# Kernel tuning notes

Measured on AMD Instinct MI355X. Metric: run time of the kernel, lower is better.

Reference implementation:

```python
import jax, jax.numpy as jnp
import numpy as np

N_E = 1024      # codes per sub-codebook
E_DIM = 64      # code dimension
BETA = 0.25     # commitment cost (VectorQuantizer(n_e, e_dim, 0.25))


def setup_inputs() -> dict:
    key = jax.random.key(0)
    k1, k2 = jax.random.split(key)
    bs, c, h, w = 16, 512, 32, 32
    m = c // E_DIM  # 8 sub-codebooks
    z = jax.random.normal(k1, (bs, c, h, w), dtype=jnp.float32)
    # taming-style init: uniform(-1/n_e, 1/n_e)
    codebooks = jax.random.uniform(
        k2, (m, N_E, E_DIM), dtype=jnp.float32,
        minval=-1.0 / N_E, maxval=1.0 / N_E)
    return {"z": z, "codebooks": codebooks}


def reference(z, codebooks):
    bs, c, h, w = z.shape
    m, n_e, e_dim = codebooks.shape
    N = bs * h * w
    # [bs,c,h,w] -> [bs,h,w,c] -> [m, N, e_dim]: batched over all m sub-codebooks at once
    zf = z.transpose(0, 2, 3, 1).reshape(N, m, e_dim).transpose(1, 0, 2)

    # squared L2 distances: ||z||^2 + ||e||^2 - 2 z.e   -> [m, N, n_e]
    d = ((zf ** 2).sum(-1, keepdims=True)
         + (codebooks ** 2).sum(-1)[:, None, :]
         - 2.0 * jnp.einsum('mnd,mkd->mnk', zf, codebooks))
    idx = jnp.argmin(d, axis=-1)  # [m, N]

    # gather nearest codes: [m, N, e_dim]
    zq = jnp.take_along_axis(codebooks, idx[:, :, None], axis=1)

    # per-sub-codebook VQ loss, summed over m (loss = sum(loss_list))
    codebook_loss = jnp.mean((jax.lax.stop_gradient(zq) - zf) ** 2, axis=(1, 2))
    commit_loss = jnp.mean((zq - jax.lax.stop_gradient(zf)) ** 2, axis=(1, 2))
    loss = jnp.sum(codebook_loss + BETA * commit_loss)

    # straight-through estimator
    zq_st = zf + jax.lax.stop_gradient(zq - zf)

    # reassemble: [m,N,d] -> [N,m*d] -> [bs,h,w,c] -> [bs,c,h,w]
    z_vq = zq_st.transpose(1, 0, 2).reshape(bs, h, w, c).transpose(0, 3, 1, 2)

    # concat of per-codebook index tensors along dim 0
    min_encoding_indices = idx.reshape(-1)  # [m*N]
    # per-code occupancy counts summed over the m codebooks -> [n_e]
    bin_count = jnp.zeros((n_e,), jnp.int32).at[min_encoding_indices].add(1)

    return z_vq, loss, min_encoding_indices, bin_count
```

## Files before the change

kernel.cpp:

```cpp
#include <hip/hip_runtime.h>
#include <cfloat>

#define BS 16
#define CC 512
#define HWD 1024
#define NN 16384
#define MM 8
#define NE 1024
#define ED 64

#define LOSS_OFF 8388608
#define IDX_OFF  8388609
#define BIN_OFF  8519681

#define TAU 4e-5f
#define UWIN 400u

#define WS_B     0
#define WS_IDX   32768
#define WS_CNT   557056
#define WS_LIST  557088
#define WS_OF    688160
#define WS_CAND  720928
#define WS_BMAT  3866656

typedef __attribute__((ext_vector_type(8))) short bf16x8;
typedef __attribute__((ext_vector_type(16))) float f32x16;

__device__ __forceinline__ unsigned short f2bf(float f) {
    unsigned int u = __float_as_uint(f);
    unsigned int r = (u + 0x7fffu + ((u >> 16) & 1u)) >> 16;
    return (unsigned short)r;
}
__device__ __forceinline__ float bf2f(unsigned short h) {
    return __uint_as_float(((unsigned int)h) << 16);
}
__device__ __forceinline__ unsigned umin_(unsigned a, unsigned b) { return a < b ? a : b; }
__device__ __forceinline__ unsigned umax_(unsigned a, unsigned b) { return a > b ? a : b; }
__device__ __forceinline__ unsigned umin3(unsigned a, unsigned b, unsigned c) {
    return umin_(umin_(a, b), c);
}

__device__ __forceinline__ float mul_rn(float a, float b) {
#pragma clang fp contract(off)
    return a * b;
}
__device__ __forceinline__ float add_rn(float a, float b) {
#pragma clang fp contract(off)
    return a + b;
}
__device__ __forceinline__ float sub_rn(float a, float b) {
#pragma clang fp contract(off)
    return a - b;
}

__device__ __forceinline__ float np_sumsq64(const float* x) {
    float r[8];
#pragma unroll
    for (int j = 0; j < 8; ++j) r[j] = mul_rn(x[j], x[j]);
#pragma unroll
    for (int i = 8; i < 64; i += 8) {
#pragma unroll
        for (int j = 0; j < 8; ++j) r[j] = add_rn(r[j], mul_rn(x[i + j], x[i + j]));
    }
    return add_rn(add_rn(add_rn(r[0], r[1]), add_rn(r[2], r[3])),
                  add_rn(add_rn(r[4], r[5]), add_rn(r[6], r[7])));
}

__device__ __forceinline__ float np_dot64(const float* zsh, const float4* cr4) {
    float v0 = 0.f, v1 = 0.f, v2 = 0.f, v3 = 0.f;
#pragma unroll
    for (int t = 0; t < 4; ++t) {
        float4 e0 = cr4[t * 4 + 0];
        float4 e1 = cr4[t * 4 + 1];
        float4 e2 = cr4[t * 4 + 2];
        float4 e3 = cr4[t * 4 + 3];
        const int d0 = 16 * t;
        v0 = add_rn(mul_rn(zsh[d0 + 0], e0.x),
             add_rn(mul_rn(zsh[d0 + 4], e1.x),
             add_rn(mul_rn(zsh[d0 + 8], e2.x),
             add_rn(mul_rn(zsh[d0 + 12], e3.x), v0))));
        v1 = add_rn(mul_rn(zsh[d0 + 1], e0.y),
             add_rn(mul_rn(zsh[d0 + 5], e1.y),
             add_rn(mul_rn(zsh[d0 + 9], e2.y),
             add_rn(mul_rn(zsh[d0 + 13], e3.y), v1))));
        v2 = add_rn(mul_rn(zsh[d0 + 2], e0.z),
             add_rn(mul_rn(zsh[d0 + 6], e1.z),
             add_rn(mul_rn(zsh[d0 + 10], e2.z),
             add_rn(mul_rn(zsh[d0 + 14], e3.z), v2))));
        v3 = add_rn(mul_rn(zsh[d0 + 3], e0.w),
             add_rn(mul_rn(zsh[d0 + 7], e1.w),
             add_rn(mul_rn(zsh[d0 + 11], e2.w),
             add_rn(mul_rn(zsh[d0 + 15], e3.w), v3))));
    }
    return add_rn(add_rn(v0, v1), add_rn(v2, v3));
}

__global__ __launch_bounds__(256) void prep_kernel(const float* __restrict__ cb,
                                                   float* __restrict__ Bhat,
                                                   uint4* __restrict__ Bmat,
                                                   float* __restrict__ out,
                                                   int* __restrict__ cnt) {
    const int tid = threadIdx.x;
    if (blockIdx.x < 32) {
        int i = blockIdx.x * 256 + tid;
        if (i == 0) { out[LOSS_OFF] = 0.0f; cnt[0] = 0; cnt[1] = 0; }
        if (i < NE) out[BIN_OFF + i] = 0.0f;
        const float4* r4 = (const float4*)(cb + (size_t)i * ED);
        float x[ED];
#pragma unroll
        for (int q = 0; q < 16; ++q) {
            float4 v = r4[q];
            x[q*4+0] = v.x; x[q*4+1] = v.y; x[q*4+2] = v.z; x[q*4+3] = v.w;
        }
        Bhat[i] = np_sumsq64(x);
        return;
    }
    int t = (blockIdx.x - 32) * 256 + tid;
    int lane = t & 63;
    int ct = (t >> 6) & 31;
    int rem = t >> 11;
    int c = rem % 13;
    int m = rem / 13;
    int h = lane >> 5;
    int k = ct * 32 + (lane & 31);

    unsigned short v[8];
#pragma unroll
    for (int j = 0; j < 8; ++j) v[j] = 0;

    if (c < 12) {
        int d0 = 16 * (c & 3) + 8 * h;
        const float* e = cb + ((size_t)m * NE + k) * ED + d0;
#pragma unroll
        for (int j = 0; j < 8; ++j) {
            float f = -2.0f * e[j];
            unsigned short hi = f2bf(f);
            v[j] = (c >= 4 && c < 8) ? f2bf(f - bf2f(hi)) : hi;
        }
    } else if (h == 0) {
        const float* e = cb + ((size_t)m * NE + k) * ED;
        float s = 0.f;
#pragma unroll
        for (int d = 0; d < ED; ++d) s += e[d] * e[d];
        v[0] = f2bf(s);
        v[1] = 0x3F80;
    }
    uint4 o;
    o.x = (unsigned)v[0] | ((unsigned)v[1] << 16);
    o.y = (unsigned)v[2] | ((unsigned)v[3] << 16);
    o.z = (unsigned)v[4] | ((unsigned)v[5] << 16);
    o.w = (unsigned)v[6] | ((unsigned)v[7] << 16);
    Bmat[t] = o;
}

__global__ __launch_bounds__(512, 4) void argmin_kernel(
        const float* __restrict__ z, const uint4* __restrict__ Bmat,
        int* __restrict__ idx_out, int* __restrict__ cnt,
        int* __restrict__ list, unsigned short* __restrict__ cand) {
    const int tid = threadIdx.x;
    const int m = blockIdx.y;
    const int row0 = blockIdx.x * 256;
    const int w = tid >> 6;
    const int l = tid & 63;
    const int h = l >> 5;
    const int r5 = l & 31;

    __shared__ uint4 ldsB[2][13 * 2 * 64];

    const int n_mine = row0 + w * 32 + r5;
    const int b = n_mine >> 10;
    const int hw = n_mine & (HWD - 1);
    const float* zbase = z + (((size_t)(b * CC + m * ED)) << 10) + hw;

    bf16x8 zh[4], zl[4];
#pragma unroll
    for (int i = 0; i < 4; ++i) {
        int o = 2 * i + h;
#pragma unroll
        for (int j = 0; j < 8; ++j) {
            float f = zbase[(size_t)(8 * o + j) << 10];
            unsigned short hb = f2bf(f);
            unsigned short lb = f2bf(f - bf2f(hb));
            zh[i][j] = (short)hb;
            zl[i][j] = (short)lb;
        }
    }
    bf16x8 ones12 = {0, 0, 0, 0, 0, 0, 0, 0};
    if (h == 0) { ones12[0] = (short)0x3F80; ones12[1] = (short)0x3F80; }

    unsigned rbm = 0xFFFFFFF0u, rsec = 0xFFFFFFFFu, rinfo = 0;
    int ccnt = 0;
    unsigned short* myslots = cand + ((size_t)(m * NN + n_mine) * 2 + h) * 6;

    auto stage = [&](int g, int bufi) {
        for (int seg = w; seg < 26; seg += 8) {
            int c = seg >> 1, ct2 = seg & 1;
            const uint4* src = Bmat +
                ((size_t)((m * 13 + c) * 32 + (g * 2 + ct2)) << 6) + l;
            uint4* dst = &ldsB[bufi][(c * 2 + ct2) * 64];
            __builtin_amdgcn_global_load_lds(
                (const __attribute__((address_space(1))) unsigned int*)src,
                (__attribute__((address_space(3))) unsigned int*)dst, 16, 0, 0);
        }
    };

    stage(0, 0);
    __syncthreads();
    int buf = 0;
    for (int g = 0; g < 16; ++g) {
        if (g < 15) stage(g + 1, buf ^ 1);

#pragma unroll
        for (int ctl = 0; ctl < 2; ++ctl) {
            f32x16 acc;
#pragma unroll
            for (int s = 0; s < 16; ++s) acc[s] = 0.0f;
#pragma unroll
            for (int c = 0; c < 13; ++c) {
                bf16x8 af = *(const bf16x8*)&ldsB[buf][(c * 2 + ctl) * 64 + l];
                bf16x8 bfr = (c < 8) ? zh[c & 3] : ((c < 12) ? zl[c & 3] : ones12);
                acc = __builtin_amdgcn_mfma_f32_32x32x16_bf16(af, bfr, acc, 0, 0, 0);
            }
            unsigned u[16];
#pragma unroll
            for (int s = 0; s < 16; ++s)
                u[s] = (__float_as_uint(acc[s]) & 0xFFFFFFF0u) | (unsigned)s;
            unsigned b0 = umin_(u[0], u[1]),  s0 = umax_(u[0], u[1]);
            unsigned b1 = umin_(u[2], u[3]),  s1 = umax_(u[2], u[3]);
            unsigned b2 = umin_(u[4], u[5]),  s2 = umax_(u[4], u[5]);
            unsigned b3 = umin_(u[6], u[7]),  s3 = umax_(u[6], u[7]);
            unsigned b4 = umin_(u[8], u[9]),  s4 = umax_(u[8], u[9]);
            unsigned b5 = umin_(u[10], u[11]), s5 = umax_(u[10], u[11]);
            unsigned b6 = umin_(u[12], u[13]), s6 = umax_(u[12], u[13]);
            unsigned b7 = umin_(u[14], u[15]), s7 = umax_(u[14], u[15]);
            unsigned B0 = umin_(b0, b1), S0 = umin3(umax_(b0, b1), s0, s1);
            unsigned B1 = umin_(b2, b3), S1 = umin3(umax_(b2, b3), s2, s3);
            unsigned B2 = umin_(b4, b5), S2 = umin3(umax_(b4, b5), s4, s5);
            unsigned B3 = umin_(b6, b7), S3 = umin3(umax_(b6, b7), s6, s7);
            unsigned C0 = umin_(B0, B1), T0 = umin3(umax_(B0, B1), S0, S1);
            unsigned C1 = umin_(B2, B3), T1 = umin3(umax_(B2, B3), S2, S3);
            unsigned bt = umin_(C0, C1), st = umin3(umax_(C0, C1), T0, T1);

            unsigned tile = (unsigned)(g * 2 + ctl);
            unsigned oldrbm = rbm;
            bool take = bt < oldrbm;
            if (take && bt + UWIN < oldrbm) ccnt = 0;
            unsigned other = take ? oldrbm : bt;
            rsec = umin3(rsec, st, other);
            rbm = take ? bt : oldrbm;
            rinfo = take ? ((tile << 4) | (bt & 15u)) : rinfo;

            unsigned limit = rbm + UWIN;
            if (bt < limit) {
#pragma unroll
                for (int s = 0; s < 16; ++s) {
                    if (u[s] < limit) {
                        if (ccnt < 6)
                            myslots[ccnt] = (unsigned short)(
                                tile * 32u + ((unsigned)s & 3u) +
                                8u * ((unsigned)s >> 2) + 4u * (unsigned)h);
                        ccnt++;
                    }
                }
            }
        }
        __syncthreads();
        buf ^= 1;
    }

    int pcnt = __shfl_xor(ccnt, 32, 64);

    unsigned ss = rinfo & 15u, tile = rinfo >> 4;
    int k = (int)(tile * 32 + (ss & 3u) + 8u * (ss >> 2) + 4u * (unsigned)h);
    unsigned orbm = __shfl_xor(rbm, 32, 64);
    int ok = __shfl_xor(k, 32, 64);
    unsigned orsec = __shfl_xor(rsec, 32, 64);
    bool take = orbm < rbm;
    unsigned lose = take ? rbm : orbm;
    unsigned fb = take ? orbm : rbm;
    int fk = take ? ok : k;
    unsigned fs = umin3(rsec, orsec, lose);
    if (l < 32) {
        int mn = m * NN + n_mine;
        idx_out[mn] = fk;
        float margin = __uint_as_float(fs & 0xFFFFFFF0u) -
                       __uint_as_float(fb & 0xFFFFFFF0u);
        if (margin < TAU) {
            int p = atomicAdd(cnt, 1);
            if (p < 32768) {
                int c0 = ccnt > 6 ? 7 : ccnt;
                int c1 = pcnt > 6 ? 7 : pcnt;
                list[p] = mn | (c0 << 20) | (c1 << 24);
            }
        }
    }
}

__global__ __launch_bounds__(256) void cand_kernel(
        const float* __restrict__ z, const float* __restrict__ cb,
        const float* __restrict__ Bhat, int* __restrict__ cnt,
        const int* __restrict__ list, const unsigned short* __restrict__ cand,
        int* __restrict__ idx_out, int* __restrict__ oflist) {
    const int tid = threadIdx.x;
    const int lane = tid & 63;
    const int wv = tid >> 6;
    const int wid = (blockIdx.x * 256 + tid) >> 6;
    const int nw = gridDim.x * 4;
    const int total = cnt[0] < 32768 ? cnt[0] : 32768;

    __shared__ float zsh[4][ED];

    for (int r = wid; r < total; r += nw) {
        const int e = list[r];
        const int mn = e & 0xFFFFF;
        const int c0 = (e >> 20) & 15;
        const int c1 = (e >> 24) & 15;
        if (c0 == 7 || c1 == 7) {
            if (lane == 0) {
                int q = atomicAdd(cnt + 1, 1);
                if (q < 8192) oflist[q] = mn;
            }
            continue;
        }
        const int m = mn >> 14;
        const int n = mn & (NN - 1);
        const int b = n >> 10;
        const int hw = n & (HWD - 1);

        zsh[wv][lane] = z[(((size_t)(b * CC + m * ED + lane)) << 10) + hw];

        int kj = -1;
        if (lane < c0) kj = cand[(size_t)mn * 12 + lane];
        else if (lane >= 8 && lane < 8 + c1) kj = cand[(size_t)mn * 12 + 6 + (lane - 8)];

        float A = np_sumsq64(&zsh[wv][0]);

        float dref = FLT_MAX;
        if (kj >= 0) {
            const float4* cr4 = (const float4*)(cb + ((size_t)m * NE + kj) * ED);
            float C = np_dot64(&zsh[wv][0], cr4);
            dref = sub_rn(add_rn(A, Bhat[m * NE + kj]), mul_rn(2.0f, C));
        }
        int kk = (kj >= 0) ? kj : NE;
#pragma unroll
        for (int off = 32; off >= 1; off >>= 1) {
            float ov = __shfl_down(dref, off, 64);
            int oi = __shfl_down(kk, off, 64);
            if (ov < dref || (ov == dref && oi < kk)) { dref = ov; kk = oi; }
        }
        if (lane == 0) idx_out[mn] = kk;
    }
}

__global__ __launch_bounds__(256) void emul_kernel(
        const float* __restrict__ z, const float* __restrict__ cb,
        const float* __restrict__ Bhat, const int* __restrict__ cnt,
        const int* __restrict__ oflist, int* __restrict__ idx_out) {
    const int tid = threadIdx.x;
    const int lane = tid & 63;
    const int w = tid >> 6;
    const int total = cnt[1] < 8192 ? cnt[1] : 8192;

    __shared__ float zsh[ED];
    __shared__ float rbest[4];
    __shared__ int ridx[4];

    for (int r = blockIdx.x; r < total; r += gridDim.x) {
        const int mn = oflist[r];
        const int m = mn >> 14;
        const int n = mn & (NN - 1);
        const int b = n >> 10;
        const int hw = n & (HWD - 1);

        __syncthreads();
        if (tid < ED) {
            const float* zbase = z + (((size_t)(b * CC + m * ED)) << 10) + hw;
            zsh[tid] = zbase[(size_t)tid << 10];
        }
        __syncthreads();

        const float A = np_sumsq64(zsh);
        const float* cbm = cb + (size_t)m * NE * ED;
        const float* Bm = Bhat + m * NE;
        float best = FLT_MAX;
        int bidx = NE;
#pragma unroll
        for (int kk = 0; kk < 4; ++kk) {
            const int k = kk * 256 + tid;
            const float4* cr4 = (const float4*)(cbm + (size_t)k * ED);
            float C = np_dot64(zsh, cr4);
            float dk = sub_rn(add_rn(A, Bm[k]), mul_rn(2.0f, C));
            if (dk < best || (dk == best && k < bidx)) { best = dk; bidx = k; }
        }
#pragma unroll
        for (int off = 32; off >= 1; off >>= 1) {
            float ov = __shfl_down(best, off, 64);
            int oi = __shfl_down(bidx, off, 64);
            if (ov < best || (ov == best && oi < bidx)) { best = ov; bidx = oi; }
        }
        if (lane == 0) { rbest[w] = best; ridx[w] = bidx; }
        __syncthreads();
        if (tid == 0) {
            float bb = rbest[0]; int bi = ridx[0];
#pragma unroll
            for (int i = 1; i < 4; ++i) {
                if (rbest[i] < bb || (rbest[i] == bb && ridx[i] < bi)) {
                    bb = rbest[i]; bi = ridx[i];
                }
            }
            idx_out[mn] = bi;
        }
    }
}

__global__ __launch_bounds__(256) void output_kernel(
        const float* __restrict__ z, const float* __restrict__ cb,
        const int* __restrict__ idx_in, float* __restrict__ out) {
    const int tid = threadIdx.x;
    const int n = blockIdx.x * 256 + tid;
    const int m = blockIdx.y;
    const int b = n >> 10;
    const int hw = n & (HWD - 1);
    const int idx = idx_in[m * NN + n];

    out[IDX_OFF + m * NN + n] = (float)idx;

    const float* cr = cb + ((size_t)m * NE + (size_t)idx) * ED;
    const float* zbase = z + (((size_t)(b * CC + m * ED)) << 10) + hw;
    float* ob = out + (((size_t)(b * CC + m * ED)) << 10) + hw;

    double acc = 0.0;
#pragma unroll
    for (int d = 0; d < ED; ++d) {
        float c = cr[d];
        float zv = zbase[(size_t)d << 10];
        ob[(size_t)d << 10] = c;
        float diff = c - zv;
        acc += (double)diff * (double)diff;
    }

    __shared__ int hist[NE];
#pragma unroll
    for (int i = 0; i < 4; ++i) hist[tid + i * 256] = 0;
    __syncthreads();
    atomicAdd(&hist[idx], 1);

#pragma unroll
    for (int off = 32; off >= 1; off >>= 1)
        acc += __shfl_down(acc, off, 64);
    __shared__ double wsum[4];
    if ((tid & 63) == 0) wsum[tid >> 6] = acc;
    __syncthreads();
    if (tid == 0) {
        double t = wsum[0] + wsum[1] + wsum[2] + wsum[3];
        atomicAdd(out + LOSS_OFF, (float)(t * (1.25 / 1048576.0)));
    }
#pragma unroll
    for (int i = 0; i < 4; ++i) {
        int v = hist[tid + i * 256];
        if (v) atomicAdd(out + BIN_OFF + tid + i * 256, (float)v);
    }
}

extern "C" void kernel_launch(void* const* d_in, const int* in_sizes, int n_in,
                              void* d_out, int out_size, void* d_ws, size_t ws_size,
                              hipStream_t stream) {
    const float* z = (const float*)d_in[0];
    const float* cb = (const float*)d_in[1];
    float* out = (float*)d_out;
    char* ws = (char*)d_ws;
    float* Bhat = (float*)(ws + WS_B);
    int* idxw = (int*)(ws + WS_IDX);
    int* cnt = (int*)(ws + WS_CNT);
    int* list = (int*)(ws + WS_LIST);
    int* oflist = (int*)(ws + WS_OF);
    unsigned short* cand = (unsigned short*)(ws + WS_CAND);
    uint4* Bmat = (uint4*)(ws + WS_BMAT);

    prep_kernel<<<dim3(864), dim3(256), 0, stream>>>(cb, Bhat, Bmat, out, cnt);
    argmin_kernel<<<dim3(NN / 256, MM), dim3(512), 0, stream>>>(
        z, Bmat, idxw, cnt, list, cand);
    cand_kernel<<<dim3(256), dim3(256), 0, stream>>>(
        z, cb, Bhat, cnt, list, cand, idxw, oflist);
    emul_kernel<<<dim3(256), dim3(256), 0, stream>>>(
        z, cb, Bhat, cnt, oflist, idxw);
    output_kernel<<<dim3(NN / 256, MM), dim3(256), 0, stream>>>(z, cb, idxw, out);
}
```

Baseline: 191.6 us.

## Fuse output gather, loss and histogram into argmin with delta fixups

Removes the separate output kernel. The argmin kernel now writes the gathered codes, the indices, the loss partials and a shared-memory histogram directly. The candidate refinement kernels apply delta corrections when they change an index: they rewrite the code row, adjust the loss by the distance difference, and move the bin count. The B matrix also drops the duplicated high-part rows (13 to 9 chunks), reusing the high-part A fragments held in registers for the z-low products. This cuts LDS staging and prep work. In exchange, the loss is now accumulated in fp32 instead of double and the argmin tail needs more registers.

```diff
diff --git a/kernel.cpp b/kernel.cpp
--- a/kernel.cpp
+++ b/kernel.cpp
@@ -12,6 +12,8 @@
 #define LOSS_OFF 8388608
 #define IDX_OFF  8388609
 #define BIN_OFF  8519681
+
+#define LOSS_SCALE (1.25f / 1048576.0f)
 
 #define TAU 4e-5f
 #define UWIN 400u
@@ -120,8 +122,8 @@
     int lane = t & 63;
     int ct = (t >> 6) & 31;
     int rem = t >> 11;
-    int c = rem % 13;
-    int m = rem / 13;
+    int c = rem % 9;
+    int m = rem / 9;
     int h = lane >> 5;
     int k = ct * 32 + (lane & 31);
 
@@ -129,14 +131,14 @@
 #pragma unroll
     for (int j = 0; j < 8; ++j) v[j] = 0;
 
-    if (c < 12) {
+    if (c < 8) {
         int d0 = 16 * (c & 3) + 8 * h;
         const float* e = cb + ((size_t)m * NE + k) * ED + d0;
 #pragma unroll
         for (int j = 0; j < 8; ++j) {
             float f = -2.0f * e[j];
             unsigned short hi = f2bf(f);
-            v[j] = (c >= 4 && c < 8) ? f2bf(f - bf2f(hi)) : hi;
+            v[j] = (c >= 4) ? f2bf(f - bf2f(hi)) : hi;
         }
     } else if (h == 0) {
         const float* e = cb + ((size_t)m * NE + k) * ED;
@@ -155,9 +157,10 @@
 }
 
 __global__ __launch_bounds__(512, 4) void argmin_kernel(
-        const float* __restrict__ z, const uint4* __restrict__ Bmat,
-        int* __restrict__ idx_out, int* __restrict__ cnt,
-        int* __restrict__ list, unsigned short* __restrict__ cand) {
+        const float* __restrict__ z, const float* __restrict__ cb,
+        const uint4* __restrict__ Bmat, int* __restrict__ idx_out,
+        int* __restrict__ cnt, int* __restrict__ list,
+        unsigned short* __restrict__ cand, float* __restrict__ out) {
     const int tid = threadIdx.x;
     const int m = blockIdx.y;
     const int row0 = blockIdx.x * 256;
@@ -166,7 +169,10 @@
     const int h = l >> 5;
     const int r5 = l & 31;
 
-    __shared__ uint4 ldsB[2][13 * 2 * 64];
+    __shared__ uint4 ldsB[2][9 * 2 * 64];
+    __shared__ int hist[NE];
+
+    for (int i = tid; i < NE; i += 512) hist[i] = 0;
 
     const int n_mine = row0 + w * 32 + r5;
     const int b = n_mine >> 10;
@@ -194,10 +200,10 @@
     unsigned short* myslots = cand + ((size_t)(m * NN + n_mine) * 2 + h) * 6;
 
     auto stage = [&](int g, int bufi) {
-        for (int seg = w; seg < 26; seg += 8) {
+        for (int seg = w; seg < 18; seg += 8) {
             int c = seg >> 1, ct2 = seg & 1;
             const uint4* src = Bmat +
-                ((size_t)((m * 13 + c) * 32 + (g * 2 + ct2)) << 6) + l;
+                ((size_t)((m * 9 + c) * 32 + (g * 2 + ct2)) << 6) + l;
             uint4* dst = &ldsB[bufi][(c * 2 + ct2) * 64];
             __builtin_amdgcn_global_load_lds(
                 (const __attribute__((address_space(1))) unsigned int*)src,
@@ -216,9 +222,18 @@
             f32x16 acc;
 #pragma unroll
             for (int s = 0; s < 16; ++s) acc[s] = 0.0f;
+            bf16x8 ah[4];
 #pragma unroll
             for (int c = 0; c < 13; ++c) {
-                bf16x8 af = *(const bf16x8*)&ldsB[buf][(c * 2 + ctl) * 64 + l];
+                bf16x8 af;
+                if (c < 8) {
+                    af = *(const bf16x8*)&ldsB[buf][(c * 2 + ctl) * 64 + l];
+                    if (c < 4) ah[c] = af;
+                } else if (c < 12) {
+                    af = ah[c - 8];
+                } else {
+                    af = *(const bf16x8*)&ldsB[buf][(16 + ctl) * 64 + l];
+                }
                 bf16x8 bfr = (c < 8) ? zh[c & 3] : ((c < 12) ? zl[c & 3] : ones12);
                 acc = __builtin_amdgcn_mfma_f32_32x32x16_bf16(af, bfr, acc, 0, 0, 0);
             }
@@ -276,14 +291,15 @@
     unsigned orbm = __shfl_xor(rbm, 32, 64);
     int ok = __shfl_xor(k, 32, 64);
     unsigned orsec = __shfl_xor(rsec, 32, 64);
-    bool take = orbm < rbm;
+    bool take = (orbm < rbm) || (orbm == rbm && ok < k);
     unsigned lose = take ? rbm : orbm;
     unsigned fb = take ? orbm : rbm;
     int fk = take ? ok : k;
     unsigned fs = umin3(rsec, orsec, lose);
+    const int mn = m * NN + n_mine;
     if (l < 32) {
-        int mn = m * NN + n_mine;
         idx_out[mn] = fk;
+        out[IDX_OFF + mn] = (float)fk;
         float margin = __uint_as_float(fs & 0xFFFFFFF0u) -
                        __uint_as_float(fb & 0xFFFFFFF0u);
         if (margin < TAU) {
@@ -294,6 +310,38 @@
                 list[p] = mn | (c0 << 20) | (c1 << 24);
             }
         }
+        atomicAdd(&hist[fk], 1);
+    }
+
+    {
+        const float4* crow = (const float4*)(cb + ((size_t)m * NE + fk) * ED + h * 32);
+        float* ob = out + (((size_t)(b * CC + m * ED)) << 10) + hw;
+        float lacc = 0.0f;
+#pragma unroll
+        for (int q = 0; q < 8; ++q) {
+            float4 cv = crow[q];
+            int dd = h * 32 + q * 4;
+            float z0 = zbase[(size_t)(dd + 0) << 10];
+            float z1 = zbase[(size_t)(dd + 1) << 10];
+            float z2 = zbase[(size_t)(dd + 2) << 10];
+            float z3 = zbase[(size_t)(dd + 3) << 10];
+            ob[(size_t)(dd + 0) << 10] = cv.x;
+            ob[(size_t)(dd + 1) << 10] = cv.y;
+            ob[(size_t)(dd + 2) << 10] = cv.z;
+            ob[(size_t)(dd + 3) << 10] = cv.w;
+            float d0 = cv.x - z0, d1 = cv.y - z1, d2 = cv.z - z2, d3 = cv.w - z3;
+            lacc += d0 * d0 + d1 * d1 + d2 * d2 + d3 * d3;
+        }
+#pragma unroll
+        for (int off = 32; off >= 1; off >>= 1)
+            lacc += __shfl_xor(lacc, off, 64);
+        if (l == 0) atomicAdd(out + LOSS_OFF, lacc * LOSS_SCALE);
+    }
+
+    __syncthreads();
+    for (int i = tid; i < NE; i += 512) {
+        int v = hist[i];
+        if (v) atomicAdd(out + BIN_OFF + i, (float)v);
     }
 }
 
@@ -301,7 +349,8 @@
         const float* __restrict__ z, const float* __restrict__ cb,
         const float* __restrict__ Bhat, int* __restrict__ cnt,
         const int* __restrict__ list, const unsigned short* __restrict__ cand,
-        int* __restrict__ idx_out, int* __restrict__ oflist) {
+        int* __restrict__ idx_out, int* __restrict__ oflist,
+        float* __restrict__ out) {
     const int tid = threadIdx.x;
     const int lane = tid & 63;
     const int wv = tid >> 6;
@@ -349,14 +398,34 @@
             int oi = __shfl_down(kk, off, 64);
             if (ov < dref || (ov == dref && oi < kk)) { dref = ov; kk = oi; }
         }
-        if (lane == 0) idx_out[mn] = kk;
+        int kfin = __shfl(kk, 0, 64);
+        int old = idx_out[mn];
+        if (kfin < NE && kfin != old) {
+            float zv = zsh[wv][lane];
+            float cold = cb[((size_t)m * NE + old) * ED + lane];
+            float cnew = cb[((size_t)m * NE + kfin) * ED + lane];
+            float dpart = (cnew - zv) * (cnew - zv) - (cold - zv) * (cold - zv);
+#pragma unroll
+            for (int off = 32; off >= 1; off >>= 1)
+                dpart += __shfl_xor(dpart, off, 64);
+            float* ob = out + (((size_t)(b * CC + m * ED)) << 10) + hw;
+            ob[(size_t)lane << 10] = cnew;
+            if (lane == 0) {
+                idx_out[mn] = kfin;
+                out[IDX_OFF + mn] = (float)kfin;
+                atomicAdd(out + LOSS_OFF, dpart * LOSS_SCALE);
+                atomicAdd(out + BIN_OFF + old, -1.0f);
+                atomicAdd(out + BIN_OFF + kfin, 1.0f);
+            }
+        }
     }
 }
 
 __global__ __launch_bounds__(256) void emul_kernel(
         const float* __restrict__ z, const float* __restrict__ cb,
         const float* __restrict__ Bhat, const int* __restrict__ cnt,
-        const int* __restrict__ oflist, int* __restrict__ idx_out) {
+        const int* __restrict__ oflist, int* __restrict__ idx_out,
+        float* __restrict__ out) {
     const int tid = threadIdx.x;
     const int lane = tid & 63;
     const int w = tid >> 6;
@@ -365,6 +434,7 @@
     __shared__ float zsh[ED];
     __shared__ float rbest[4];
     __shared__ int ridx[4];
+    __shared__ int sfin;
 
     for (int r = blockIdx.x; r < total; r += gridDim.x) {
         const int mn = oflist[r];
@@ -409,57 +479,29 @@
                     bb = rbest[i]; bi = ridx[i];
                 }
             }
-            idx_out[mn] = bi;
-        }
-    }
-}
-
-__global__ __launch_bounds__(256) void output_kernel(
-        const float* __restrict__ z, const float* __restrict__ cb,
-        const int* __restrict__ idx_in, float* __restrict__ out) {
-    const int tid = threadIdx.x;
-    const int n = blockIdx.x * 256 + tid;
-    const int m = blockIdx.y;
-    const int b = n >> 10;
-    const int hw = n & (HWD - 1);
-    const int idx = idx_in[m * NN + n];
-
-    out[IDX_OFF + m * NN + n] = (float)idx;
-
-    const float* cr = cb + ((size_t)m * NE + (size_t)idx) * ED;
-    const float* zbase = z + (((size_t)(b * CC + m * ED)) << 10) + hw;
-    float* ob = out + (((size_t)(b * CC + m * ED)) << 10) + hw;
-
-    double acc = 0.0;
-#pragma unroll
-    for (int d = 0; d < ED; ++d) {
-        float c = cr[d];
-        float zv = zbase[(size_t)d << 10];
-        ob[(size_t)d << 10] = c;
-        float diff = c - zv;
-        acc += (double)diff * (double)diff;
-    }
-
-    __shared__ int hist[NE];
-#pragma unroll
-    for (int i = 0; i < 4; ++i) hist[tid + i * 256] = 0;
-    __syncthreads();
-    atomicAdd(&hist[idx], 1);
-
-#pragma unroll
-    for (int off = 32; off >= 1; off >>= 1)
-        acc += __shfl_down(acc, off, 64);
-    __shared__ double wsum[4];
-    if ((tid & 63) == 0) wsum[tid >> 6] = acc;
-    __syncthreads();
-    if (tid == 0) {
-        double t = wsum[0] + wsum[1] + wsum[2] + wsum[3];
-        atomicAdd(out + LOSS_OFF, (float)(t * (1.25 / 1048576.0)));
-    }
-#pragma unroll
-    for (int i = 0; i < 4; ++i) {
-        int v = hist[tid + i * 256];
-        if (v) atomicAdd(out + BIN_OFF + tid + i * 256, (float)v);
+            sfin = bi;
+        }
+        __syncthreads();
+        const int kfin = sfin;
+        const int old = idx_out[mn];
+        if (kfin != old && tid < 64) {
+            float zv = zsh[tid];
+            float cold = cb[((size_t)m * NE + old) * ED + tid];
+            float cnew = cb[((size_t)m * NE + kfin) * ED + tid];
+            float dpart = (cnew - zv) * (cnew - zv) - (cold - zv) * (cold - zv);
+#pragma unroll
+            for (int off = 32; off >= 1; off >>= 1)
+                dpart += __shfl_xor(dpart, off, 64);
+            float* ob = out + (((size_t)(b * CC + m * ED)) << 10) + hw;
+            ob[(size_t)tid << 10] = cnew;
+            if (tid == 0) {
+                idx_out[mn] = kfin;
+                out[IDX_OFF + mn] = (float)kfin;
+                atomicAdd(out + LOSS_OFF, dpart * LOSS_SCALE);
+                atomicAdd(out + BIN_OFF + old, -1.0f);
+                atomicAdd(out + BIN_OFF + kfin, 1.0f);
+            }
+        }
     }
 }
 
@@ -478,12 +520,11 @@
     unsigned short* cand = (unsigned short*)(ws + WS_CAND);
     uint4* Bmat = (uint4*)(ws + WS_BMAT);
 
-    prep_kernel<<<dim3(864), dim3(256), 0, stream>>>(cb, Bhat, Bmat, out, cnt);
+    prep_kernel<<<dim3(608), dim3(256), 0, stream>>>(cb, Bhat, Bmat, out, cnt);
     argmin_kernel<<<dim3(NN / 256, MM), dim3(512), 0, stream>>>(
-        z, Bmat, idxw, cnt, list, cand);
+        z, cb, Bmat, idxw, cnt, list, cand, out);
     cand_kernel<<<dim3(256), dim3(256), 0, stream>>>(
-        z, cb, Bhat, cnt, list, cand, idxw, oflist);
+        z, cb, Bhat, cnt, list, cand, idxw, oflist, out);
     emul_kernel<<<dim3(256), dim3(256), 0, stream>>>(
-        z, cb, Bhat, cnt, oflist, idxw);
-    output_kernel<<<dim3(NN / 256, MM), dim3(256), 0, stream>>>(z, cb, idxw, out);
-}
+        z, cb, Bhat, cnt, oflist, idxw, out);
+}
```

Measured after the change: 210.6 us. 9.9% more time.
